# Optimization experiments

Hardware: AMD Instinct MI355X
Metric: run time of the kernel (lower is better)

The kernel has to match this reference:

```python
import jax, jax.numpy as jnp
import numpy as np

T, B, I, H, O = 512, 64, 256, 1024, 256


def setup_inputs() -> dict:
    key = jax.random.key(0)
    ks = jax.random.split(key, 7)
    s_ih = 1.0 / np.sqrt(H)
    return {
        "x": jax.random.normal(ks[0], (T, B, I), dtype=jnp.float32),
        "W_ih": jax.random.uniform(ks[1], (4 * H, I), jnp.float32, -s_ih, s_ih),
        "W_hh": jax.random.uniform(ks[2], (4 * H, H), jnp.float32, -s_ih, s_ih),
        "b_ih": jax.random.uniform(ks[3], (4 * H,), jnp.float32, -s_ih, s_ih),
        "b_hh": jax.random.uniform(ks[4], (4 * H,), jnp.float32, -s_ih, s_ih),
        "W_out": jax.random.uniform(ks[5], (O, H), jnp.float32, -s_ih, s_ih),
        "b_out": jax.random.uniform(ks[6], (O,), jnp.float32, -s_ih, s_ih),
    }


def reference(x, W_ih, W_hh, b_ih, b_hh, W_out, b_out):
    # x: [T, B, I]. PyTorch LSTM gate order: i, f, g, o.
    hdim = W_hh.shape[1]
    # Precompute input contribution to gates for all timesteps: [T, B, 4H]
    xg = jnp.einsum("tbi,gi->tbg", x, W_ih) + b_ih + b_hh

    def step(carry, xt):
        h, c = carry
        gates = xt + h @ W_hh.T  # [B, 4H]
        i_g, f_g, g_g, o_g = jnp.split(gates, 4, axis=-1)
        i_g = jax.nn.sigmoid(i_g)
        f_g = jax.nn.sigmoid(f_g)
        g_g = jnp.tanh(g_g)
        o_g = jax.nn.sigmoid(o_g)
        c = f_g * c + i_g * g_g
        h = o_g * jnp.tanh(c)
        return (h, c), h

    b = x.shape[1]
    h0 = jnp.zeros((b, hdim), x.dtype)
    c0 = jnp.zeros((b, hdim), x.dtype)
    _, hs = jax.lax.scan(step, (h0, c0), xg)  # hs: [T, B, H]
    return hs @ W_out.T + b_out  # [T, B, O]
```

## Files before the change

kernel.cpp:

```cpp
#include <hip/hip_runtime.h>

#define T_ 512
#define B_ 64
#define I_ 256
#define H_ 1024
#define G4_ 4096
#define O_ 256

#define NBLK 256
#define NTHR 512

typedef short bfrag8 __attribute__((ext_vector_type(8)));
typedef float f32x4 __attribute__((ext_vector_type(4)));
typedef unsigned int u32;

__device__ __forceinline__ unsigned short f2bf(float f) {
    unsigned int u = __builtin_bit_cast(unsigned int, f);
    u = (u + 0x7fffu + ((u >> 16) & 1u)) >> 16;
    return (unsigned short)u;
}

__device__ __forceinline__ float sigmoid_fast(float x) {
    return 1.0f / (1.0f + __expf(-x));
}
__device__ __forceinline__ float tanh_fast(float x) {
    x = fminf(fmaxf(x, -15.0f), 15.0f);
    float e = __expf(2.0f * x);
    return (e - 1.0f) / (e + 1.0f);
}

__device__ __forceinline__ void store_wt_u32(u32* p, u32 v) {
    asm volatile("global_store_dword %0, %1, off sc0 sc1" :: "v"(p), "v"(v) : "memory");
}
__device__ __forceinline__ void poll2_u32(const u32* p0, const u32* p1, u32& a, u32& b) {
    asm volatile("global_load_dword %0, %2, off sc0 sc1\n\t"
                 "global_load_dword %1, %3, off sc0 sc1\n\t"
                 "s_waitcnt vmcnt(0)"
                 : "=&v"(a), "=&v"(b) : "v"(p0), "v"(p1) : "memory");
}

__global__ void cvt_bf16(const float* __restrict__ in, unsigned short* __restrict__ out, int n) {
    int i = blockIdx.x * blockDim.x + threadIdx.x;
    int st = gridDim.x * blockDim.x;
    for (; i < n; i += st) out[i] = f2bf(in[i]);
}

__global__ void bias_sum_k(const float* __restrict__ a, const float* __restrict__ b,
                           float* __restrict__ o, int n) {
    int i = blockIdx.x * blockDim.x + threadIdx.x;
    if (i < n) o[i] = a[i] + b[i];
}

__global__ __launch_bounds__(NTHR, 2) void lstm_persist(
    const unsigned short* __restrict__ xbf,
    const unsigned short* __restrict__ whh,
    const unsigned short* __restrict__ wih,
    const float* __restrict__ bsum,
    unsigned short* __restrict__ hs,
    u32* __restrict__ flg)
{
    __shared__ float glp[2][32][33];

    const int bid = blockIdx.x;
    const int gid = bid >> 7;
    const int lb  = bid & 127;
    const int cg0 = lb * 8;
    const int gb0 = gid * 32;
    const int tid = threadIdx.x;
    const int w   = tid >> 6;
    const int l   = tid & 63;
    const int l16 = l & 15;
    const int lk8 = (l >> 4) << 3;
    const int p     = w & 3;
    const int mtile = p >> 1;
    const int ntile = p & 1;
    const int khalf = w >> 2;

    const int nrow = ntile * 16 + l16;
    const int grow = (nrow >> 3) * 1024 + cg0 + (nrow & 7);
    const int arow = gb0 + mtile * 16 + l16;

    bfrag8 wh[16];
    bfrag8 wx[4];
    {
        const unsigned short* wp = whh + (size_t)grow * H_ + khalf * 512 + lk8;
        #pragma unroll
        for (int kt = 0; kt < 16; ++kt) wh[kt] = *(const bfrag8*)(wp + kt * 32);
        const unsigned short* xp = wih + (size_t)grow * I_ + khalf * 128 + lk8;
        #pragma unroll
        for (int kt = 0; kt < 4; ++kt) wx[kt] = *(const bfrag8*)(xp + kt * 32);
    }

    const int pb  = tid >> 2;
    const int pjp = (tid & 3) * 2;
    float c0 = 0.f, c1 = 0.f;
    float bias_g[4][2];
    if (tid < 128) {
        #pragma unroll
        for (int g = 0; g < 4; ++g) {
            bias_g[g][0] = bsum[g * 1024 + cg0 + pjp];
            bias_g[g][1] = bsum[g * 1024 + cg0 + pjp + 1];
        }
    }

    u32* myflag = flg + (gid * 128 + lb) * 16;
    const u32* pf0 = flg + (gid * 128 + l) * 16;
    const u32* pf1 = flg + (gid * 128 + l + 64) * 16;

    const int mrow = (l >> 4) * 4;

    __syncthreads();

    for (int t = 0; t < T_; ++t) {
        f32x4 accA = {0.f, 0.f, 0.f, 0.f};
        f32x4 accB = {0.f, 0.f, 0.f, 0.f};

        {
            const unsigned short* ap =
                xbf + (size_t)t * (B_ * I_) + (size_t)arow * I_ + khalf * 128 + lk8;
            #pragma unroll
            for (int kt = 0; kt < 4; ++kt) {
                bfrag8 a = *(const bfrag8*)(ap + kt * 32);
                accA = __builtin_amdgcn_mfma_f32_16x16x32_bf16(a, wx[kt], accA, 0, 0, 0);
            }
        }

        if (t > 0) {
            if (w == 0) {
                const u32 tgt = (u32)t;
                while (true) {
                    u32 a, b;
                    poll2_u32(pf0, pf1, a, b);
                    if (__all(a >= tgt && b >= tgt)) break;
                    __builtin_amdgcn_s_sleep(1);
                }
            }
            __syncthreads();

            const unsigned short* ap = hs + (size_t)(t - 1) * (B_ * H_) +
                                       (size_t)arow * H_ + khalf * 512 + lk8;
            #pragma unroll
            for (int kt = 0; kt < 8; ++kt) {
                bfrag8 a = *(const bfrag8*)(ap + kt * 32);
                accA = __builtin_amdgcn_mfma_f32_16x16x32_bf16(a, wh[kt], accA, 0, 0, 0);
            }
            #pragma unroll
            for (int kt = 8; kt < 16; ++kt) {
                bfrag8 a = *(const bfrag8*)(ap + kt * 32);
                accB = __builtin_amdgcn_mfma_f32_16x16x32_bf16(a, wh[kt], accB, 0, 0, 0);
            }
        }

        #pragma unroll
        for (int r = 0; r < 4; ++r)
            glp[khalf][mtile * 16 + mrow + r][ntile * 16 + l16] = accA[r] + accB[r];
        __syncthreads();

        if (tid < 128) {
            float pre[4][2];
            #pragma unroll
            for (int g = 0; g < 4; ++g) {
                int n = g * 8 + pjp;
                pre[g][0] = glp[0][pb][n]     + glp[1][pb][n]     + bias_g[g][0];
                pre[g][1] = glp[0][pb][n + 1] + glp[1][pb][n + 1] + bias_g[g][1];
            }
            float i0 = sigmoid_fast(pre[0][0]), i1 = sigmoid_fast(pre[0][1]);
            float f0 = sigmoid_fast(pre[1][0]), f1 = sigmoid_fast(pre[1][1]);
            float g0 = tanh_fast(pre[2][0]),    g1 = tanh_fast(pre[2][1]);
            float o0 = sigmoid_fast(pre[3][0]), o1 = sigmoid_fast(pre[3][1]);
            c0 = f0 * c0 + i0 * g0;
            c1 = f1 * c1 + i1 * g1;
            float h0 = o0 * tanh_fast(c0);
            float h1 = o1 * tanh_fast(c1);
            u32 hv = ((u32)f2bf(h1) << 16) | (u32)f2bf(h0);
            u32* hp = (u32*)(hs + (size_t)t * (B_ * H_) +
                             (size_t)(gb0 + pb) * H_ + cg0 + pjp);
            store_wt_u32(hp, hv);
            asm volatile("s_waitcnt vmcnt(0)" ::: "memory");
        }
        __syncthreads();

        if (tid == 0) store_wt_u32(myflag, (u32)(t + 1));
    }
}

__global__ __launch_bounds__(256) void out_gemm(
    const unsigned short* __restrict__ hs,
    const unsigned short* __restrict__ wout,
    const float* __restrict__ bout,
    float* __restrict__ out)
{
    const int bid  = blockIdx.x;
    const int nblk = bid & 3;
    const int mblk = bid >> 2;
    const int tid  = threadIdx.x;
    const int w    = tid >> 6;
    const int l    = tid & 63;
    const int l16  = l & 15;
    const int lk8  = (l >> 4) << 3;

    const int m0 = mblk * 64 + w * 16;
    const int n0 = nblk * 64;

    f32x4 acc[4] = {};
    const unsigned short* __restrict__ arow = hs + (size_t)(m0 + l16) * H_;
#pragma unroll 2
    for (int kt = 0; kt < 32; ++kt) {
        int k = kt * 32 + lk8;
        bfrag8 af = *(const bfrag8*)(arow + k);
#pragma unroll
        for (int nt = 0; nt < 4; ++nt) {
            bfrag8 bf = *(const bfrag8*)(wout + (size_t)(n0 + nt * 16 + l16) * H_ + k);
            acc[nt] = __builtin_amdgcn_mfma_f32_16x16x32_bf16(af, bf, acc[nt], 0, 0, 0);
        }
    }
    const int mrow = (l >> 4) * 4;
#pragma unroll
    for (int nt = 0; nt < 4; ++nt) {
        int o = n0 + nt * 16 + l16;
        float bb = bout[o];
#pragma unroll
        for (int r = 0; r < 4; ++r) {
            out[(size_t)(m0 + mrow + r) * O_ + o] = acc[nt][r] + bb;
        }
    }
}

extern "C" void kernel_launch(void* const* d_in, const int* in_sizes, int n_in,
                              void* d_out, int out_size, void* d_ws, size_t ws_size,
                              hipStream_t stream) {
    const float* x     = (const float*)d_in[0];
    const float* W_ih  = (const float*)d_in[1];
    const float* W_hh  = (const float*)d_in[2];
    const float* b_ih  = (const float*)d_in[3];
    const float* b_hh  = (const float*)d_in[4];
    const float* W_out = (const float*)d_in[5];
    const float* b_out = (const float*)d_in[6];
    float* out = (float*)d_out;

    char* ws = (char*)d_ws;
    unsigned short* hs   = (unsigned short*)(ws);
    unsigned short* xbf  = (unsigned short*)(ws + 67108864);
    unsigned short* whh  = (unsigned short*)(ws + 83886080);
    unsigned short* wih  = (unsigned short*)(ws + 92274688);
    unsigned short* wout = (unsigned short*)(ws + 94371840);
    float*          bsum = (float*)         (ws + 94896128);
    u32*            flg  = (u32*)           (ws + 94912512);

    cvt_bf16<<<2048, 256, 0, stream>>>(x,     xbf,  T_ * B_ * I_);
    cvt_bf16<<<2048, 256, 0, stream>>>(W_hh,  whh,  G4_ * H_);
    cvt_bf16<<<1024, 256, 0, stream>>>(W_ih,  wih,  G4_ * I_);
    cvt_bf16<<<256,  256, 0, stream>>>(W_out, wout, O_ * H_);
    bias_sum_k<<<16, 256, 0, stream>>>(b_ih, b_hh, bsum, G4_);
    hipMemsetAsync(flg, 0, 16384, stream);

    void* args[] = {(void*)&xbf, (void*)&whh, (void*)&wih, (void*)&bsum,
                    (void*)&hs, (void*)&flg};
    hipLaunchCooperativeKernel((const void*)lstm_persist, dim3(NBLK), dim3(NTHR),
                               args, 0, stream);

    out_gemm<<<2048, 256, 0, stream>>>(hs, wout, b_out, out);
}
```

Before: 3.737 ms.

## Replace per-block flags with striped atomic counters and drop end-of-step block barrier

Swaps the per-block step flags for four striped atomic counters per batch group. Each writer wavefront increments a counter after its h store, and waiters poll a single counter per lane until it reaches 64*t. This removes the trailing __syncthreads and the per-block flag store, and cuts the number of polled addresses from 128 to 4. It also pins the weight fragment loads with inline asm so the compiler keeps them in registers. The costs are atomic contention on a few cache lines and correctness that depends on counting writer waves exactly.

```diff
diff --git a/kernel.cpp b/kernel.cpp
--- a/kernel.cpp
+++ b/kernel.cpp
@@ -32,11 +32,17 @@
 __device__ __forceinline__ void store_wt_u32(u32* p, u32 v) {
     asm volatile("global_store_dword %0, %1, off sc0 sc1" :: "v"(p), "v"(v) : "memory");
 }
-__device__ __forceinline__ void poll2_u32(const u32* p0, const u32* p1, u32& a, u32& b) {
-    asm volatile("global_load_dword %0, %2, off sc0 sc1\n\t"
-                 "global_load_dword %1, %3, off sc0 sc1\n\t"
+__device__ __forceinline__ u32 poll1_u32(const u32* p) {
+    u32 v;
+    asm volatile("global_load_dword %0, %1, off sc0 sc1\n\t"
                  "s_waitcnt vmcnt(0)"
-                 : "=&v"(a), "=&v"(b) : "v"(p0), "v"(p1) : "memory");
+                 : "=&v"(v) : "v"(p) : "memory");
+    return v;
+}
+__device__ __forceinline__ bfrag8 pin_load_frag(const unsigned short* p) {
+    bfrag8 r;
+    asm volatile("global_load_dwordx4 %0, %1, off" : "=&v"(r) : "v"(p));
+    return r;
 }
 
 __global__ void cvt_bf16(const float* __restrict__ in, unsigned short* __restrict__ out, int n) {
@@ -57,7 +63,7 @@
     const unsigned short* __restrict__ wih,
     const float* __restrict__ bsum,
     unsigned short* __restrict__ hs,
-    u32* __restrict__ flg)
+    u32* __restrict__ cnt)
 {
     __shared__ float glp[2][32][33];
 
@@ -85,10 +91,12 @@
     {
         const unsigned short* wp = whh + (size_t)grow * H_ + khalf * 512 + lk8;
         #pragma unroll
-        for (int kt = 0; kt < 16; ++kt) wh[kt] = *(const bfrag8*)(wp + kt * 32);
+        for (int kt = 0; kt < 16; ++kt) wh[kt] = pin_load_frag(wp + kt * 32);
         const unsigned short* xp = wih + (size_t)grow * I_ + khalf * 128 + lk8;
         #pragma unroll
-        for (int kt = 0; kt < 4; ++kt) wx[kt] = *(const bfrag8*)(xp + kt * 32);
+        for (int kt = 0; kt < 4; ++kt) wx[kt] = pin_load_frag(xp + kt * 32);
+        asm volatile("s_waitcnt vmcnt(0)" ::: "memory");
+        __builtin_amdgcn_sched_barrier(0);
     }
 
     const int pb  = tid >> 2;
@@ -103,9 +111,8 @@
         }
     }
 
-    u32* myflag = flg + (gid * 128 + lb) * 16;
-    const u32* pf0 = flg + (gid * 128 + l) * 16;
-    const u32* pf1 = flg + (gid * 128 + l + 64) * 16;
+    u32* mycnt = cnt + (gid * 4 + (lb & 3)) * 16;
+    const u32* pollp = cnt + (gid * 4 + (l & 3)) * 16;
 
     const int mrow = (l >> 4) * 4;
 
@@ -127,11 +134,10 @@
 
         if (t > 0) {
             if (w == 0) {
-                const u32 tgt = (u32)t;
+                const u32 tgt = 64u * (u32)t;
                 while (true) {
-                    u32 a, b;
-                    poll2_u32(pf0, pf1, a, b);
-                    if (__all(a >= tgt && b >= tgt)) break;
+                    u32 v = poll1_u32(pollp);
+                    if (__all(v >= tgt)) break;
                     __builtin_amdgcn_s_sleep(1);
                 }
             }
@@ -177,10 +183,10 @@
                              (size_t)(gb0 + pb) * H_ + cg0 + pjp);
             store_wt_u32(hp, hv);
             asm volatile("s_waitcnt vmcnt(0)" ::: "memory");
-        }
-        __syncthreads();
-
-        if (tid == 0) store_wt_u32(myflag, (u32)(t + 1));
+            if ((tid & 63) == 0)
+                __hip_atomic_fetch_add(mycnt, 1u, __ATOMIC_RELAXED,
+                                       __HIP_MEMORY_SCOPE_AGENT);
+        }
     }
 }
 
@@ -245,17 +251,17 @@
     unsigned short* wih  = (unsigned short*)(ws + 92274688);
     unsigned short* wout = (unsigned short*)(ws + 94371840);
     float*          bsum = (float*)         (ws + 94896128);
-    u32*            flg  = (u32*)           (ws + 94912512);
+    u32*            cnt  = (u32*)           (ws + 94912512);
 
     cvt_bf16<<<2048, 256, 0, stream>>>(x,     xbf,  T_ * B_ * I_);
     cvt_bf16<<<2048, 256, 0, stream>>>(W_hh,  whh,  G4_ * H_);
     cvt_bf16<<<1024, 256, 0, stream>>>(W_ih,  wih,  G4_ * I_);
     cvt_bf16<<<256,  256, 0, stream>>>(W_out, wout, O_ * H_);
     bias_sum_k<<<16, 256, 0, stream>>>(b_ih, b_hh, bsum, G4_);
-    hipMemsetAsync(flg, 0, 16384, stream);
+    hipMemsetAsync(cnt, 0, 512, stream);
 
     void* args[] = {(void*)&xbf, (void*)&whh, (void*)&wih, (void*)&bsum,
-                    (void*)&hs, (void*)&flg};
+                    (void*)&hs, (void*)&cnt};
     hipLaunchCooperativeKernel((const void*)lstm_persist, dim3(NBLK), dim3(NTHR),
                                args, 0, stream);
 
```

Result: faster. 3.644 ms (-2.5%).
